# Performance work log

Hardware: AMD Instinct MI355X
Metric: run time of the kernel (lower is better)

Reference implementation:

```python
import jax, jax.numpy as jnp
import numpy as np

B, E, P, S = 64, 512, 31, 200  # batch, emitters, patch size, canvas size
HALF = 15  # patch half-width; slice is x-15 : x+16


def setup_inputs() -> dict:
    key = jax.random.key(0)
    k1, k2, k3 = jax.random.split(key, 3)
    images4D = jax.random.normal(k1, (B, E, P, P), dtype=jnp.float32)
    # x,y must be in [15, 184] so the 31x31 patch stays inside the 200x200 canvas
    xy = jax.random.randint(k2, (B, E, 2), HALF, S - HALF, dtype=jnp.int32)
    z = jax.random.randint(k3, (B, E, 1), 0, 100, dtype=jnp.int32)
    xyz = jnp.concatenate([xy, z], axis=-1)  # [B, E, 3] int32
    return {"images4D": images4D, "xyz": xyz}


def reference(images4D, xyz):
    Bn, En, H, W = images4D.shape
    off = jnp.arange(H, dtype=jnp.int32) - HALF          # [-15 .. 15]
    rows = xyz[:, :, 0:1].astype(jnp.int32) + off        # [B, E, 31]
    cols = xyz[:, :, 1:2].astype(jnp.int32) + off        # [B, E, 31]
    # flat canvas index for every patch pixel: [B, E, 31, 31]
    idx = rows[:, :, :, None] * S + cols[:, :, None, :]

    def per_batch(idx_b, patch_b):
        # single fused scatter-add of all emitters' patches into one canvas
        return jnp.zeros(S * S, dtype=patch_b.dtype).at[idx_b.ravel()].add(patch_b.ravel())

    img = jax.vmap(per_batch)(idx, images4D)              # [B, S*S]
    return img.reshape(Bn, 1, S, S)
```

## Files before the change

kernel.cpp:

```cpp
#include <hip/hip_runtime.h>

constexpr int B    = 64;
constexpr int E    = 512;
constexpr int P    = 31;
constexpr int S    = 200;
constexpr int HALF = 15;

constexpr int TS     = 16;
constexpr int NTD    = (S + TS - 1) / TS;
constexpr int NTILES = NTD * NTD;
constexpr int NBINS  = B * NTILES;
constexpr int CAP    = 128;

constexpr int THREADS = 256;
constexpr int NW      = THREADS / 64;
constexpr int NXCD    = 8;

__global__ __launch_bounds__(E)
void imgs4dto3d_bin_kernel(const int* __restrict__ xyz,
                           int*       __restrict__ counts,
                           unsigned*  __restrict__ entries)
{
    __shared__ int cnt[NTILES];

    const int b = blockIdx.x;
    const int e = threadIdx.x;

    for (int i = e; i < NTILES; i += E) cnt[i] = 0;
    __syncthreads();

    const int x = xyz[(size_t)(b * E + e) * 3 + 0];
    const int y = xyz[(size_t)(b * E + e) * 3 + 1];
    const unsigned pk = (unsigned)e | ((unsigned)x << 9) | ((unsigned)y << 17);

    const int tr_lo = (x - HALF) >> 4, tr_hi = (x + HALF) >> 4;
    const int tc_lo = (y - HALF) >> 4, tc_hi = (y + HALF) >> 4;

    for (int tr = tr_lo; tr <= tr_hi; ++tr) {
        for (int tc = tc_lo; tc <= tc_hi; ++tc) {
            const int t   = tr * NTD + tc;
            const int pos = atomicAdd(&cnt[t], 1);
            if (pos < CAP)
                entries[(size_t)(b * NTILES + t) * CAP + pos] = pk;
        }
    }
    __syncthreads();

    for (int i = e; i < NTILES; i += E)
        counts[b * NTILES + i] = cnt[i];
}

__global__ __launch_bounds__(THREADS)
void imgs4dto3d_gather_kernel(const float*    __restrict__ img,
                              const int*      __restrict__ counts,
                              const unsigned* __restrict__ entries,
                              float*          __restrict__ out)
{
    const int wgid = blockIdx.x;
    const int xcd  = wgid & (NXCD - 1);
    const int seq  = wgid >> 3;
    const int b    = ((seq / NTILES) << 3) | xcd;
    const int t    = seq % NTILES;

    const int tid  = threadIdx.x;
    const int wid  = tid >> 6;
    const int lane = tid & 63;

    const int tr = t / NTD;
    const int tc = t % NTD;
    const int r0 = tr * TS;
    const int c0 = tc * TS;

    const int col  = lane & 15;
    const int rowg = lane >> 4;
    const int c    = c0 + col;

    const int rr = r0 + rowg * 4 + HALF;
    const int cc = c + HALF;

    const int bin = b * NTILES + t;
    const int n   = min(counts[bin], CAP);
    const int qsz = ((n + NW * 4 - 1) / (NW * 4)) * 4;
    const int lo  = min(n, wid * qsz);
    const int hi  = min(n, lo + qsz);

    const uint4* lst = reinterpret_cast<const uint4*>(entries + (size_t)bin * CAP);

    float a0 = 0.f, a1 = 0.f, a2 = 0.f, a3 = 0.f;
    const float* imgb = img + (size_t)b * E * (P * P);

    for (int i = lo; i < hi; i += 8) {
        const uint4 ea = lst[i >> 2];
        const uint4 eb = ((i + 4) < hi) ? lst[(i >> 2) + 1] : ea;
        const unsigned pks[8] = {ea.x, ea.y, ea.z, ea.w, eb.x, eb.y, eb.z, eb.w};

        float v[8][4];
        #pragma unroll
        for (int u = 0; u < 8; ++u) {
            const bool inb = (i + u) < hi;
            const unsigned pk = pks[u];
            const int e = (int)(pk & 511u);
            const int x = (int)((pk >> 9) & 255u);
            const int y = (int)(pk >> 17);

            const int pc  = cc - y;
            const int pr0 = rr - x;
            const bool colok = inb && ((unsigned)pc <= 30u);
            const float* bp = imgb + (size_t)e * (P * P) + pr0 * P + pc;
            #pragma unroll
            for (int q = 0; q < 4; ++q) {
                const bool kq = colok && ((unsigned)(pr0 + q) <= 30u);
                v[u][q] = kq ? bp[P * q] : 0.f;
            }
        }
        #pragma unroll
        for (int u = 0; u < 8; ++u) {
            a0 += v[u][0]; a1 += v[u][1]; a2 += v[u][2]; a3 += v[u][3];
        }
    }

    __shared__ float part[NW * THREADS];
    part[wid * THREADS + 0 * 64 + lane] = a0;
    part[wid * THREADS + 1 * 64 + lane] = a1;
    part[wid * THREADS + 2 * 64 + lane] = a2;
    part[wid * THREADS + 3 * 64 + lane] = a3;
    __syncthreads();

    const int q     = tid >> 6;
    const int lane2 = tid & 63;
    const int row   = r0 + ((lane2 >> 4) << 2) + q;
    const int cst   = c0 + (lane2 & 15);
    const float v = part[0 * THREADS + tid] + part[1 * THREADS + tid] +
                    part[2 * THREADS + tid] + part[3 * THREADS + tid];
    if (row < S && cst < S) {
        out[(size_t)b * (S * S) + row * S + cst] = v;
    }
}

extern "C" void kernel_launch(void* const* d_in, const int* in_sizes, int n_in,
                              void* d_out, int out_size, void* d_ws, size_t ws_size,
                              hipStream_t stream)
{
    const float* img = (const float*)d_in[0];
    const int*   xyz = (const int*)d_in[1];
    float*       out = (float*)d_out;

    int*      counts  = (int*)d_ws;
    unsigned* entries = (unsigned*)d_ws + NBINS;

    imgs4dto3d_bin_kernel<<<B, E, 0, stream>>>(xyz, counts, entries);

    imgs4dto3d_gather_kernel<<<NBINS, THREADS, 0, stream>>>(img, counts, entries, out);
}
```

Before: 36.04 us.

## Store bin count in entry header and interleave entry groups across waves

Moves each tile's count into the first uint4 of its entry list, so the gather kernel reads count and first entries together with no dependent load. Entries are now split across waves round-robin in groups of four rather than in contiguous chunks, and the first two groups are loaded up front. This removes the serial count-then-list load latency at each block's start. In exchange, per-bin capacity drops by four entries, and the speculative preloads read slots that may never have been written, which are masked out.

```diff
diff --git a/kernel.cpp b/kernel.cpp
--- a/kernel.cpp
+++ b/kernel.cpp
@@ -11,6 +11,7 @@
 constexpr int NTILES = NTD * NTD;
 constexpr int NBINS  = B * NTILES;
 constexpr int CAP    = 128;
+constexpr int ECAP   = CAP - 4;
 
 constexpr int THREADS = 256;
 constexpr int NW      = THREADS / 64;
@@ -18,7 +19,6 @@
 
 __global__ __launch_bounds__(E)
 void imgs4dto3d_bin_kernel(const int* __restrict__ xyz,
-                           int*       __restrict__ counts,
                            unsigned*  __restrict__ entries)
 {
     __shared__ int cnt[NTILES];
@@ -40,19 +40,18 @@
         for (int tc = tc_lo; tc <= tc_hi; ++tc) {
             const int t   = tr * NTD + tc;
             const int pos = atomicAdd(&cnt[t], 1);
-            if (pos < CAP)
-                entries[(size_t)(b * NTILES + t) * CAP + pos] = pk;
+            if (pos < ECAP)
+                entries[(size_t)(b * NTILES + t) * CAP + 4 + pos] = pk;
         }
     }
     __syncthreads();
 
     for (int i = e; i < NTILES; i += E)
-        counts[b * NTILES + i] = cnt[i];
+        entries[(size_t)(b * NTILES + i) * CAP] = (unsigned)cnt[i];
 }
 
 __global__ __launch_bounds__(THREADS)
 void imgs4dto3d_gather_kernel(const float*    __restrict__ img,
-                              const int*      __restrict__ counts,
                               const unsigned* __restrict__ entries,
                               float*          __restrict__ out)
 {
@@ -66,6 +65,13 @@
     const int wid  = tid >> 6;
     const int lane = tid & 63;
 
+    const int bin = b * NTILES + t;
+    const uint4* lst4 = reinterpret_cast<const uint4*>(entries + (size_t)bin * CAP);
+
+    const uint4 hdr = lst4[0];
+    const uint4 g0  = lst4[1 + wid];
+    const uint4 g1  = lst4[5 + wid];
+
     const int tr = t / NTD;
     const int tc = t % NTD;
     const int r0 = tr * TS;
@@ -78,26 +84,18 @@
     const int rr = r0 + rowg * 4 + HALF;
     const int cc = c + HALF;
 
-    const int bin = b * NTILES + t;
-    const int n   = min(counts[bin], CAP);
-    const int qsz = ((n + NW * 4 - 1) / (NW * 4)) * 4;
-    const int lo  = min(n, wid * qsz);
-    const int hi  = min(n, lo + qsz);
-
-    const uint4* lst = reinterpret_cast<const uint4*>(entries + (size_t)bin * CAP);
+    const int n = min((int)hdr.x, ECAP);
 
     float a0 = 0.f, a1 = 0.f, a2 = 0.f, a3 = 0.f;
     const float* imgb = img + (size_t)b * E * (P * P);
 
-    for (int i = lo; i < hi; i += 8) {
-        const uint4 ea = lst[i >> 2];
-        const uint4 eb = ((i + 4) < hi) ? lst[(i >> 2) + 1] : ea;
-        const unsigned pks[8] = {ea.x, ea.y, ea.z, ea.w, eb.x, eb.y, eb.z, eb.w};
-
+    auto process8 = [&](uint4 ga, uint4 gb, int jb0, int jb1) {
+        const unsigned pks[8] = {ga.x, ga.y, ga.z, ga.w, gb.x, gb.y, gb.z, gb.w};
         float v[8][4];
         #pragma unroll
         for (int u = 0; u < 8; ++u) {
-            const bool inb = (i + u) < hi;
+            const int j = ((u < 4) ? jb0 : jb1) + (u & 3);
+            const bool inb = j < n;
             const unsigned pk = pks[u];
             const int e = (int)(pk & 511u);
             const int x = (int)((pk >> 9) & 255u);
@@ -117,6 +115,14 @@
         for (int u = 0; u < 8; ++u) {
             a0 += v[u][0]; a1 += v[u][1]; a2 += v[u][2]; a3 += v[u][3];
         }
+    };
+
+    process8(g0, g1, 4 * wid, 4 * wid + 16);
+
+    for (int k = 2; 4 * wid + 16 * k < n; k += 2) {
+        const uint4 ga = lst4[1 + wid + 4 * k];
+        const uint4 gb = lst4[min(1 + wid + 4 * (k + 1), CAP / 4 - 1)];
+        process8(ga, gb, 4 * wid + 16 * k, 4 * wid + 16 * (k + 1));
     }
 
     __shared__ float part[NW * THREADS];
@@ -145,10 +151,9 @@
     const int*   xyz = (const int*)d_in[1];
     float*       out = (float*)d_out;
 
-    int*      counts  = (int*)d_ws;
-    unsigned* entries = (unsigned*)d_ws + NBINS;
+    unsigned* entries = (unsigned*)d_ws;
 
-    imgs4dto3d_bin_kernel<<<B, E, 0, stream>>>(xyz, counts, entries);
+    imgs4dto3d_bin_kernel<<<B, E, 0, stream>>>(xyz, entries);
 
-    imgs4dto3d_gather_kernel<<<NBINS, THREADS, 0, stream>>>(img, counts, entries, out);
+    imgs4dto3d_gather_kernel<<<NBINS, THREADS, 0, stream>>>(img, entries, out);
 }
```

Result: slower. 38.39 us (+6.5%).
